# Kernel optimization log

Hardware: AMD Instinct MI355X
Metric: run time of the kernel (lower is better)

The kernel has to match this reference:

```python
import jax, jax.numpy as jnp
import numpy as np

B, S, D = 2, 2048, 2048
H = 16
Q_LORA = 1024
KV_LORA = 512
NOPE = 128
ROPE = 64
VH = 128
QK = NOPE + ROPE
EPS = 1e-3
SCALE = QK ** -0.5


def rms_norm(x, w):
    x32 = x.astype(jnp.float32)
    n = x32 * jax.lax.rsqrt(jnp.mean(x32 * x32, axis=-1, keepdims=True) + EPS)
    return w * n.astype(x.dtype)


def apply_rope(x, cos, sin):
    # x: [b, s, h, d]; cos/sin: [1, s, 1, d//2].
    # torch view_as_complex pairs consecutive elements: (x0,x1),(x2,x3),...
    xr, xi = x[..., 0::2], x[..., 1::2]
    yr = xr * cos - xi * sin
    yi = xr * sin + xi * cos
    return jnp.stack([yr, yi], axis=-1).reshape(x.shape)


def setup_inputs() -> dict:
    key = jax.random.key(0)
    ks = jax.random.split(key, 8)

    def lin(k, out, inn):
        bound = 1.0 / float(np.sqrt(inn))
        return jax.random.uniform(k, (out, inn), jnp.float32, -bound, bound)

    inv_freq = 1.0 / (10000.0 ** (np.arange(0, ROPE, 2, dtype=np.float32) / ROPE))
    ang = np.arange(S, dtype=np.float32)[:, None] * inv_freq[None, :]  # [S, ROPE/2]
    return {
        "x": jax.random.normal(ks[0], (B, S, D), jnp.float32),
        "start_pos": 0,
        "cos": jnp.asarray(np.cos(ang), jnp.float32),
        "sin": jnp.asarray(np.sin(ang), jnp.float32),
        "wq_a_w": lin(ks[1], Q_LORA, D),
        "wq_a_b": jnp.zeros((Q_LORA,), jnp.float32),
        "q_norm_w": jnp.ones((Q_LORA,), jnp.float32),
        "wq_b_w": lin(ks[2], H * QK, Q_LORA),
        "wq_b_b": jnp.zeros((H * QK,), jnp.float32),
        "wkv_a_w": lin(ks[3], KV_LORA + ROPE, D),
        "wkv_a_b": jnp.zeros((KV_LORA + ROPE,), jnp.float32),
        "kv_norm_w": jnp.ones((KV_LORA,), jnp.float32),
        "wkv_b_w": lin(ks[4], H * (NOPE + VH), KV_LORA),
        "wo_w": lin(ks[5], D, H * VH),
        "wo_b": jnp.zeros((D,), jnp.float32),
    }


def reference(x, start_pos, cos, sin, wq_a_w, wq_a_b, q_norm_w, wq_b_w, wq_b_b,
              wkv_a_w, wkv_a_b, kv_norm_w, wkv_b_w, wo_w, wo_b):
    b, s, _ = x.shape
    cos_ = cos[None, :, None, :]
    sin_ = sin[None, :, None, :]

    # q path: low-rank down-proj, RMSNorm, up-proj
    q = rms_norm(x @ wq_a_w.T + wq_a_b, q_norm_w) @ wq_b_w.T + wq_b_b
    q = q.reshape(b, s, H, QK)
    q_nope, q_pe = q[..., :NOPE], q[..., NOPE:]
    q_pe = apply_rope(q_pe, cos_, sin_)

    # kv path: joint low-rank latent + rope key
    kv_full = x @ wkv_a_w.T + wkv_a_b
    kv, k_pe = kv_full[..., :KV_LORA], kv_full[..., KV_LORA:]
    k_pe = apply_rope(k_pe[:, :, None, :], cos_, sin_)[:, :, 0, :]  # [b, t, ROPE]

    wkv_b = wkv_b_w.reshape(H, NOPE + VH, KV_LORA)
    # absorb k up-projection into q (MLA trick): q_nope -> latent space
    q_nope = jnp.einsum('bshd,hdc->bshc', q_nope, wkv_b[:, :NOPE])  # [b,s,H,KV_LORA]

    kv_c = rms_norm(kv, kv_norm_w)  # latent KV cache contents [b, t, KV_LORA]

    scores = (jnp.einsum('bshc,btc->bsht', q_nope, kv_c)
              + jnp.einsum('bshr,btr->bsht', q_pe, k_pe)) * SCALE
    # NOTE: source builds a causal mask but never adds it -> plain softmax (faithful)
    probs = jax.nn.softmax(scores.astype(jnp.float32), axis=-1).astype(x.dtype)

    o = jnp.einsum('bsht,btc->bshc', probs, kv_c)          # latent output
    o = jnp.einsum('bshc,hdc->bshd', o, wkv_b[:, NOPE:])    # v up-projection
    return o.reshape(b, s, H * VH) @ wo_w.T + wo_b
```

## Files before the change

### kernel.cpp

```cpp
#include <hip/hip_runtime.h>
#include <stdint.h>

typedef uint16_t u16;
typedef __bf16 bf16x8 __attribute__((ext_vector_type(8)));
typedef float f32x4 __attribute__((ext_vector_type(4)));
typedef u16 u16x8 __attribute__((ext_vector_type(8)));

#define EPS 1e-3f
#define SCALE_F 0.07216878364870323f
#define THR_RAW 110.0f

__device__ __forceinline__ float bf2f(u16 u) {
    union { uint32_t i; float f; } v; v.i = ((uint32_t)u) << 16; return v.f;
}
__device__ __forceinline__ u16 f2bf(float f) {
    union { float f; uint32_t i; } v; v.f = f;
    uint32_t x = v.i;
    return (u16)((x + 0x7fffu + ((x >> 16) & 1u)) >> 16);
}

__device__ __forceinline__ void async_cp16(const u16* g, u16* l) {
    __builtin_amdgcn_global_load_lds(
        (const __attribute__((address_space(1))) uint32_t*)g,
        (__attribute__((address_space(3))) uint32_t*)l,
        16, 0, 0);
}

struct Cvt {
    const void* src[14];
    u16* dst[14];
    long off[15];
};

__global__ __launch_bounds__(256) void cvt_kernel(Cvt c, const uint32_t* qnw_u32, long total8)
{
    const long i8 = (long)blockIdx.x * 256 + threadIdx.x;
    if (i8 >= total8) return;
    const long e = i8 * 8;
    const bool is_f32 = (qnw_u32[0] == 0x3F800000u);
    int t = 0;
    while (e >= c.off[t + 1]) ++t;
    const long local = e - c.off[t];
    u16* d = c.dst[t] + local;
    if (is_f32) {
        const float* s = (const float*)c.src[t] + local;
        const f32x4 a = *(const f32x4*)s;
        const f32x4 b = *(const f32x4*)(s + 4);
        u16x8 o;
        #pragma unroll
        for (int j = 0; j < 4; ++j) { o[j] = f2bf(a[j]); o[j + 4] = f2bf(b[j]); }
        *(u16x8*)d = o;
    } else {
        *(u16x8*)d = *(const u16x8*)((const u16*)c.src[t] + local);
    }
}

struct GemmP {
    const u16* A; const u16* B; const u16* bias; u16* C;
    int M, N, K, lda, ldb, ldc; float alpha; int c_f32;
    int z0, hcnt;
    long sAl, sAb, sAh, sBl, sBb, sBh, sCl, sCb, sCh;
    int gx, gy;
};

__device__ __forceinline__ void gemm_body(
    u16* As, u16* Bs, int bx, int by, int bz, const GemmP& p)
{
    const u16* A = p.A; const u16* B = p.B; const u16* bias = p.bias;
    u16* C = p.C;
    const int N = p.N, K = p.K, lda = p.lda, ldb = p.ldb, ldc = p.ldc;

    const int zg = p.z0 + bz;
    const int zb = zg / p.hcnt, zh = zg - zb * p.hcnt;
    A += (long)bz * p.sAl + (long)zb * p.sAb + (long)zh * p.sAh;
    B += (long)bz * p.sBl + (long)zb * p.sBb + (long)zh * p.sBh;
    C += (long)bz * p.sCl + (long)zb * p.sCb + (long)zh * p.sCh;

    const int tid  = threadIdx.x;
    const int wave = tid >> 6, lane = tid & 63;
    const int wm = (wave >> 1) << 6, wn = (wave & 1) << 6;
    const int quad = lane >> 4, r15 = lane & 15;

    const int tileM = by * 128;
    const int tileN = bx * 128;

    const u16* Ag[4]; const u16* Bg[4];
    u16* lA[4]; u16* lB[4];
    #pragma unroll
    for (int i = 0; i < 4; ++i) {
        const int cc = i * 256 + tid;
        const int rA = cc >> 3, kb = (cc & 7) << 3;
        int rB = tileN + rA; if (rB > N - 1) rB = N - 1;
        Ag[i] = A + (long)(tileM + rA) * lda + kb;
        Bg[i] = B + (long)rB * ldb + kb;
        lA[i] = &As[cc << 3];
        lB[i] = &Bs[cc << 3];
    }

    f32x4 acc[4][4] = {};

    const u16* aRd[4]; const u16* bRd[4];
    #pragma unroll
    for (int i = 0; i < 4; ++i) {
        aRd[i] = &As[(wm + i * 16 + r15) * 64 + quad * 8];
        bRd[i] = &Bs[(wn + i * 16 + r15) * 64 + quad * 8];
    }

    for (int k0 = 0; k0 < K; k0 += 64) {
        #pragma unroll
        for (int i = 0; i < 4; ++i) {
            async_cp16(Ag[i], lA[i]);
            async_cp16(Bg[i], lB[i]);
            Ag[i] += 64; Bg[i] += 64;
        }
        __syncthreads();
        #pragma unroll
        for (int kk = 0; kk < 2; ++kk) {
            bf16x8 af[4], bfr[4];
            #pragma unroll
            for (int i = 0; i < 4; ++i) {
                af[i]  = *(const bf16x8*)(aRd[i] + kk * 32);
                bfr[i] = *(const bf16x8*)(bRd[i] + kk * 32);
            }
            #pragma unroll
            for (int mi = 0; mi < 4; ++mi)
                #pragma unroll
                for (int ni = 0; ni < 4; ++ni)
                    acc[mi][ni] = __builtin_amdgcn_mfma_f32_16x16x32_bf16(
                        af[mi], bfr[ni], acc[mi][ni], 0, 0, 0);
        }
        __syncthreads();
    }

    #pragma unroll
    for (int mi = 0; mi < 4; ++mi) {
        const int row = tileM + wm + mi * 16 + quad * 4;
        #pragma unroll
        for (int ni = 0; ni < 4; ++ni) {
            const int col = tileN + wn + ni * 16 + r15;
            if (col < N) {
                if (p.c_f32) {
                    const float bv = bias ? bf2f(bias[col]) : 0.f;
                    #pragma unroll
                    for (int r = 0; r < 4; ++r)
                        ((float*)C)[(long)(row + r) * ldc + col] =
                            acc[mi][ni][r] * p.alpha + bv;
                } else {
                    #pragma unroll
                    for (int r = 0; r < 4; ++r) {
                        u16 t = f2bf(acc[mi][ni][r] * p.alpha);
                        if (bias) t = f2bf(bf2f(t) + bf2f(bias[col]));
                        C[(long)(row + r) * ldc + col] = t;
                    }
                }
            }
        }
    }
}

__global__ __launch_bounds__(256) void gemm_bt_kernel(GemmP p)
{
    __shared__ u16 As[128 * 64];
    __shared__ u16 Bs[128 * 64];
    gemm_body(As, Bs, blockIdx.x, blockIdx.y, blockIdx.z, p);
}

__global__ __launch_bounds__(256) void gemm_tri_kernel(
    GemmP pa, GemmP pb, GemmP pc, int na, int nb)
{
    __shared__ u16 As[128 * 64];
    __shared__ u16 Bs[128 * 64];
    int bid = blockIdx.x;
    if (bid < na) {
        const int bx = bid % pa.gx; const int rem = bid / pa.gx;
        gemm_body(As, Bs, bx, rem % pa.gy, rem / pa.gy, pa);
    } else if (bid < na + nb) {
        bid -= na;
        const int bx = bid % pb.gx; const int rem = bid / pb.gx;
        gemm_body(As, Bs, bx, rem % pb.gy, rem / pb.gy, pb);
    } else {
        bid -= na + nb;
        const int bx = bid % pc.gx; const int rem = bid / pc.gx;
        gemm_body(As, Bs, bx, rem % pc.gy, rem / pc.gy, pc);
    }
}

#define PS 72

__global__ __launch_bounds__(256, 2) void flash_kernel(
    const u16* __restrict__ q, const u16* __restrict__ K2,
    const u16* __restrict__ Vt, u16* __restrict__ O,
    const u16* __restrict__ cosb, const u16* __restrict__ sinb)
{
    __shared__ __align__(16) u16 Ks[64 * 192];
    __shared__ __align__(16) u16 Vs[128 * 64];
    __shared__ __align__(16) u16 Ps[4][32 * PS];

    const int bid = blockIdx.x;
    const int xcd = bid & 7;
    const int idx = bid >> 3;
    const int bh  = xcd * 4 + (idx >> 4);
    const int mt  = idx & 15;
    const int b = bh >> 4, h = bh & 15;

    const int tid = threadIdx.x;
    const int wave = tid >> 6, lane = tid & 63;
    const int quad = lane >> 4, r15 = lane & 15;
    const int r7 = r15 & 7;

    const long qrow0 = (long)b * 2048 + mt * 128 + wave * 32;
    u16* myPs = Ps[wave];

    bf16x8 qf[2][6];
    #pragma unroll
    for (int mi = 0; mi < 2; ++mi) {
        const u16* qp = q + (qrow0 + mi * 16 + r15) * 3072 + h * 192 + quad * 8;
        #pragma unroll
        for (int kst = 0; kst < 4; ++kst)
            qf[mi][kst] = *(const bf16x8*)(qp + kst * 32);
        const int srow = mt * 128 + wave * 32 + mi * 16 + r15;
        #pragma unroll
        for (int kst = 4; kst < 6; ++kst) {
            const u16x8 v = *(const u16x8*)(qp + kst * 32);
            u16x8 o;
            const int jj0 = (kst - 4) * 16 + quad * 4;
            #pragma unroll
            for (int pp = 0; pp < 4; ++pp) {
                const float xr = bf2f(v[2 * pp]), xi = bf2f(v[2 * pp + 1]);
                const float c  = bf2f(cosb[(long)srow * 32 + jj0 + pp]);
                const float si = bf2f(sinb[(long)srow * 32 + jj0 + pp]);
                o[2 * pp]     = f2bf(bf2f(f2bf(xr * c))  - bf2f(f2bf(xi * si)));
                o[2 * pp + 1] = f2bf(bf2f(f2bf(xr * si)) + bf2f(f2bf(xi * c)));
            }
            qf[mi][kst] = *(const bf16x8*)&o;
        }
    }

    f32x4 Oacc[2][8] = {};
    float m_i[2][4], l_i[2][4];
    #pragma unroll
    for (int mi = 0; mi < 2; ++mi)
        #pragma unroll
        for (int r = 0; r < 4; ++r) { m_i[mi][r] = -1e30f; l_i[mi][r] = 0.f; }

    const u16* Kbh = K2 + (long)b * 2048 * 3072 + h * 192;
    const u16* Vbh = Vt + (long)bh * 128 * 2048;

    const u16* gK[6];
    #pragma unroll
    for (int i = 0; i < 6; ++i) {
        const int c = i * 256 + tid;
        const int row = c / 24, s = c - row * 24;
        gK[i] = Kbh + (long)row * 3072 + ((s ^ (row & 7)) << 3);
    }
    const u16* gV[4];
    #pragma unroll
    for (int i = 0; i < 4; ++i) {
        const int c = i * 256 + tid;
        const int d = c >> 3, s = c & 7;
        gV[i] = Vbh + (long)d * 2048 + ((s ^ (d & 7)) << 3);
    }

    #pragma unroll
    for (int i = 0; i < 6; ++i) {
        async_cp16(gK[i], &Ks[(i * 256 + tid) << 3]);
        gK[i] += 64 * 3072;
    }
    __syncthreads();

    for (int j = 0; j < 32; ++j) {
        #pragma unroll
        for (int i = 0; i < 4; ++i) {
            async_cp16(gV[i], &Vs[(i * 256 + tid) << 3]);
            gV[i] += 64;
        }

        f32x4 S[2][4] = {};
        __builtin_amdgcn_s_setprio(1);
        #pragma unroll
        for (int kst = 0; kst < 6; ++kst) {
            bf16x8 bfr[4];
            #pragma unroll
            for (int ni = 0; ni < 4; ++ni)
                bfr[ni] = *(const bf16x8*)&Ks[(ni * 16 + r15) * 192
                                              + (((kst * 4 + quad) ^ r7) << 3)];
            #pragma unroll
            for (int mi = 0; mi < 2; ++mi)
                #pragma unroll
                for (int ni = 0; ni < 4; ++ni)
                    S[mi][ni] = __builtin_amdgcn_mfma_f32_16x16x32_bf16(
                        qf[mi][kst], bfr[ni], S[mi][ni], 0, 0, 0);
        }
        __builtin_amdgcn_s_setprio(0);

        __syncthreads();

        #pragma unroll
        for (int i = 0; i < 6; ++i) {
            async_cp16(gK[i], &Ks[(i * 256 + tid) << 3]);
            gK[i] += 64 * 3072;
        }

        float tmax[2][4];
        float gmax = -1e30f;
        #pragma unroll
        for (int mi = 0; mi < 2; ++mi)
            #pragma unroll
            for (int r = 0; r < 4; ++r) {
                float t = S[mi][0][r];
                #pragma unroll
                for (int ni = 1; ni < 4; ++ni) t = fmaxf(t, S[mi][ni][r]);
                t = fmaxf(t, __shfl_xor(t, 1, 16));
                t = fmaxf(t, __shfl_xor(t, 2, 16));
                t = fmaxf(t, __shfl_xor(t, 4, 16));
                t = fmaxf(t, __shfl_xor(t, 8, 16));
                tmax[mi][r] = t;
                gmax = fmaxf(gmax, t - m_i[mi][r]);
            }
        if (!__all(gmax <= THR_RAW)) {
            #pragma unroll
            for (int mi = 0; mi < 2; ++mi)
                #pragma unroll
                for (int r = 0; r < 4; ++r) {
                    const float mnew = fmaxf(m_i[mi][r], tmax[mi][r]);
                    const float al = __expf((m_i[mi][r] - mnew) * SCALE_F);
                    m_i[mi][r] = mnew;
                    l_i[mi][r] *= al;
                    #pragma unroll
                    for (int ni = 0; ni < 8; ++ni) Oacc[mi][ni][r] *= al;
                }
        }
        #pragma unroll
        for (int mi = 0; mi < 2; ++mi)
            #pragma unroll
            for (int r = 0; r < 4; ++r) {
                const int lrow = mi * 16 + quad * 4 + r;
                const float mm = m_i[mi][r];
                float ps = 0.f;
                #pragma unroll
                for (int ni = 0; ni < 4; ++ni) {
                    const float pv = __expf((S[mi][ni][r] - mm) * SCALE_F);
                    ps += pv;
                    myPs[lrow * PS + ni * 16 + r15] = f2bf(pv);
                }
                ps += __shfl_xor(ps, 1, 16);
                ps += __shfl_xor(ps, 2, 16);
                ps += __shfl_xor(ps, 4, 16);
                ps += __shfl_xor(ps, 8, 16);
                l_i[mi][r] += ps;
            }

        __builtin_amdgcn_s_setprio(1);
        #pragma unroll
        for (int kst = 0; kst < 2; ++kst) {
            bf16x8 af[2], bv[8];
            #pragma unroll
            for (int mi = 0; mi < 2; ++mi)
                af[mi] = *(const bf16x8*)&myPs[(mi * 16 + r15) * PS
                                               + kst * 32 + quad * 8];
            #pragma unroll
            for (int ni = 0; ni < 8; ++ni)
                bv[ni] = *(const bf16x8*)&Vs[(ni * 16 + r15) * 64
                                             + (((kst * 4 + quad) ^ r7) << 3)];
            #pragma unroll
            for (int mi = 0; mi < 2; ++mi)
                #pragma unroll
                for (int ni = 0; ni < 8; ++ni)
                    Oacc[mi][ni] = __builtin_amdgcn_mfma_f32_16x16x32_bf16(
                        af[mi], bv[ni], Oacc[mi][ni], 0, 0, 0);
        }
        __builtin_amdgcn_s_setprio(0);

        __syncthreads();
    }

    #pragma unroll
    for (int mi = 0; mi < 2; ++mi)
        #pragma unroll
        for (int r = 0; r < 4; ++r) {
            const float inv = 1.f / l_i[mi][r];
            const long row = qrow0 + mi * 16 + quad * 4 + r;
            #pragma unroll
            for (int ni = 0; ni < 8; ++ni)
                O[row * 2048 + h * 128 + ni * 16 + r15] =
                    f2bf(Oacc[mi][ni][r] * inv);
        }
}

__global__ __launch_bounds__(256) void norm_kv_kernel(
    const u16* __restrict__ cosb, const u16* __restrict__ sinb,
    const u16* __restrict__ qnw, const u16* __restrict__ kvnw,
    u16* __restrict__ comb, u16* __restrict__ K2)
{
    __shared__ float sm[4];
    __shared__ u16 rp[64];
    const int bid = blockIdx.x;
    const int tid = threadIdx.x;
    if (bid < 4096) {
        u16* xr = comb + (long)bid * 1600;
        float v[4];
        float ss = 0.f;
        #pragma unroll
        for (int i = 0; i < 4; ++i) { v[i] = bf2f(xr[tid + (i << 8)]); ss += v[i] * v[i]; }
        for (int o = 32; o; o >>= 1) ss += __shfl_xor(ss, o, 64);
        if ((tid & 63) == 0) sm[tid >> 6] = ss;
        __syncthreads();
        const float rinv = rsqrtf((sm[0] + sm[1] + sm[2] + sm[3]) / 1024.f + EPS);
        #pragma unroll
        for (int i = 0; i < 4; ++i) {
            const u16 nb = f2bf(v[i] * rinv);
            xr[tid + (i << 8)] = f2bf(bf2f(qnw[tid + (i << 8)]) * bf2f(nb));
        }
    } else {
        const long bs = bid - 4096;
        const int s = (int)(bs & 2047);
        u16* io = comb + bs * 1600 + 1024;
        const float v0 = bf2f(io[tid * 2]), v1 = bf2f(io[tid * 2 + 1]);
        float ss = v0 * v0 + v1 * v1;
        for (int off = 32; off; off >>= 1) ss += __shfl_xor(ss, off, 64);
        if ((tid & 63) == 0) sm[tid >> 6] = ss;
        __syncthreads();
        const float rinv = rsqrtf((sm[0] + sm[1] + sm[2] + sm[3]) / 512.f + EPS);
        const u16 n0 = f2bf(v0 * rinv), n1 = f2bf(v1 * rinv);
        io[tid * 2]     = f2bf(bf2f(kvnw[tid * 2]) * bf2f(n0));
        io[tid * 2 + 1] = f2bf(bf2f(kvnw[tid * 2 + 1]) * bf2f(n1));
        if (tid < 32) {
            const int j = tid;
            const float xr = bf2f(io[512 + 2 * j]), xi = bf2f(io[512 + 2 * j + 1]);
            const float c = bf2f(cosb[s * 32 + j]), si = bf2f(sinb[s * 32 + j]);
            rp[2 * j]     = f2bf(bf2f(f2bf(xr * c))  - bf2f(f2bf(xi * si)));
            rp[2 * j + 1] = f2bf(bf2f(f2bf(xr * si)) + bf2f(f2bf(xi * c)));
        }
        __syncthreads();
        #pragma unroll
        for (int i = 0; i < 4; ++i) {
            const int slot = tid + (i << 8);
            const int h = slot >> 6, r = slot & 63;
            K2[bs * 3072 + h * 192 + 128 + r] = rp[r];
        }
    }
}

extern "C" void kernel_launch(void* const* d_in, const int* in_sizes, int n_in,
                              void* d_out, int out_size, void* d_ws, size_t ws_size,
                              hipStream_t stream)
{
    float* out = (float*)d_out;

    char* p = (char*)d_ws;
    auto alloc = [&](size_t elems) { u16* r = (u16*)p; p += elems * 2; return r; };
    u16* c_cos  = alloc(65536);
    u16* c_sin  = alloc(65536);
    u16* c_wqa  = alloc(2097152);
    u16* c_wkva = alloc(1179648);
    u16* c_wqab = alloc(1024);
    u16* c_wkvab= alloc(576);
    u16* c_qnw  = alloc(1024);
    u16* c_wqb  = alloc(3145728);
    u16* c_wqbb = alloc(3072);
    u16* c_kvnw = alloc(512);
    u16* c_wkvb = alloc(2097152);
    u16* c_wo   = alloc(4194304);
    u16* c_wob  = alloc(2048);
    u16* q    = alloc(4096UL * 3072);
    u16* K2   = alloc(4096UL * 3072);
    u16* O    = alloc(4096UL * 2048);
    u16* comb = alloc(4096UL * 1600);
    u16* xb = (u16*)d_out;
    u16* Vt = (u16*)d_out + 8388608;

    Cvt cv;
    const long sizes[14] = {8388608, 65536, 65536, 2097152, 1024, 1024, 3145728,
                            3072, 1179648, 576, 512, 2097152, 4194304, 2048};
    u16* dsts[14] = {xb, c_cos, c_sin, c_wqa, c_wqab, c_qnw, c_wqb, c_wqbb,
                     c_wkva, c_wkvab, c_kvnw, c_wkvb, c_wo, c_wob};
    const int srcidx[14] = {0, 2, 3, 4, 5, 6, 7, 8, 9, 10, 11, 12, 13, 14};
    long acc_off = 0;
    for (int t = 0; t < 14; ++t) {
        cv.src[t] = d_in[srcidx[t]];
        cv.dst[t] = dsts[t];
        cv.off[t] = acc_off;
        acc_off += sizes[t];
    }
    cv.off[14] = acc_off;
    const long total8 = acc_off / 8;
    cvt_kernel<<<dim3((unsigned)((total8 + 255) / 256)), dim3(256), 0, stream>>>(
        cv, (const uint32_t*)d_in[6], total8);

    auto mkp = [&](const u16* A, const u16* B, const u16* bias, u16* C,
                   int M, int N, int K, int lda, int ldb, int ldc, float alpha,
                   int c_f32, int z0, int hcnt,
                   long sAl, long sAb, long sAh,
                   long sBl, long sBb, long sBh,
                   long sCl, long sCb, long sCh) {
        GemmP g;
        g.A = A; g.B = B; g.bias = bias; g.C = C;
        g.M = M; g.N = N; g.K = K; g.lda = lda; g.ldb = ldb; g.ldc = ldc;
        g.alpha = alpha; g.c_f32 = c_f32; g.z0 = z0; g.hcnt = hcnt;
        g.sAl = sAl; g.sAb = sAb; g.sAh = sAh;
        g.sBl = sBl; g.sBb = sBb; g.sBh = sBh;
        g.sCl = sCl; g.sCb = sCb; g.sCh = sCh;
        g.gx = (N + 127) / 128; g.gy = M / 128;
        return g;
    };
    auto gemm = [&](const GemmP& g, int nz) {
        gemm_bt_kernel<<<dim3(g.gx, g.gy, nz), dim3(256), 0, stream>>>(g);
    };

    gemm(mkp(xb, c_wqa, c_wqab, comb, 4096, 1600, 2048, 2048, 2048, 1600, 1.f, 0,
             0, 1, 0, 0, 0, 0, 0, 0, 0, 0, 0), 1);
    norm_kv_kernel<<<dim3(8192), dim3(256), 0, stream>>>(
        c_cos, c_sin, c_qnw, c_kvnw, comb, K2);
    {
        GemmP pq = mkp(comb, c_wqb, c_wqbb, q,
                       4096, 3072, 1024, 1600, 1024, 3072, 1.f, 0,
                       0, 1, 0, 0, 0, 0, 0, 0, 0, 0, 0);
        GemmP pk = mkp(comb + 1024, c_wkvb, nullptr, K2,
                       4096, 128, 512, 1600, 512, 3072, 1.f, 0,
                       0, 16, 0, 0, 0, 0, 0, 256L * 512, 0, 0, 192);
        pk.gx = 1; pk.gy = 32;
        GemmP pv = mkp(c_wkvb + 128 * 512, comb + 1024, nullptr, Vt,
                       128, 2048, 512, 512, 1600, 2048, 1.f, 0,
                       0, 16,
                       0, 0, 256L * 512,
                       0, 2048L * 1600, 0,
                       0, 16L * 128 * 2048, 128L * 2048);
        pv.gx = 16; pv.gy = 1;
        gemm_tri_kernel<<<dim3(1792), dim3(256), 0, stream>>>(pq, pk, pv, 768, 512);
    }
    flash_kernel<<<dim3(512), dim3(256), 0, stream>>>(q, K2, Vt, O, c_cos, c_sin);
    gemm(mkp(O, c_wo, c_wob, (u16*)out, 4096, 2048, 2048, 2048, 2048, 2048, 1.f, 1,
             0, 1, 0, 0, 0, 0, 0, 0, 0, 0, 0), 1);
}
```

Before: 500.2 us.

## Split flash attention work across 8 waves with 16 query rows each

```diff
diff --git a/kernel.cpp b/kernel.cpp
--- a/kernel.cpp
+++ b/kernel.cpp
@@ -187,14 +187,14 @@
 
 #define PS 72
 
-__global__ __launch_bounds__(256, 2) void flash_kernel(
+__global__ __launch_bounds__(512, 4) void flash_kernel(
     const u16* __restrict__ q, const u16* __restrict__ K2,
     const u16* __restrict__ Vt, u16* __restrict__ O,
     const u16* __restrict__ cosb, const u16* __restrict__ sinb)
 {
     __shared__ __align__(16) u16 Ks[64 * 192];
     __shared__ __align__(16) u16 Vs[128 * 64];
-    __shared__ __align__(16) u16 Ps[4][32 * PS];
+    __shared__ __align__(16) u16 Ps[8][16 * PS];
 
     const int bid = blockIdx.x;
     const int xcd = bid & 7;
@@ -208,17 +208,16 @@
     const int quad = lane >> 4, r15 = lane & 15;
     const int r7 = r15 & 7;
 
-    const long qrow0 = (long)b * 2048 + mt * 128 + wave * 32;
+    const long qrow0 = (long)b * 2048 + mt * 128 + wave * 16;
     u16* myPs = Ps[wave];
 
-    bf16x8 qf[2][6];
-    #pragma unroll
-    for (int mi = 0; mi < 2; ++mi) {
-        const u16* qp = q + (qrow0 + mi * 16 + r15) * 3072 + h * 192 + quad * 8;
+    bf16x8 qf[6];
+    {
+        const u16* qp = q + (qrow0 + r15) * 3072 + h * 192 + quad * 8;
         #pragma unroll
         for (int kst = 0; kst < 4; ++kst)
-            qf[mi][kst] = *(const bf16x8*)(qp + kst * 32);
-        const int srow = mt * 128 + wave * 32 + mi * 16 + r15;
+            qf[kst] = *(const bf16x8*)(qp + kst * 32);
+        const int srow = mt * 128 + wave * 16 + r15;
         #pragma unroll
         for (int kst = 4; kst < 6; ++kst) {
             const u16x8 v = *(const u16x8*)(qp + kst * 32);
@@ -232,50 +231,48 @@
                 o[2 * pp]     = f2bf(bf2f(f2bf(xr * c))  - bf2f(f2bf(xi * si)));
                 o[2 * pp + 1] = f2bf(bf2f(f2bf(xr * si)) + bf2f(f2bf(xi * c)));
             }
-            qf[mi][kst] = *(const bf16x8*)&o;
-        }
-    }
-
-    f32x4 Oacc[2][8] = {};
-    float m_i[2][4], l_i[2][4];
-    #pragma unroll
-    for (int mi = 0; mi < 2; ++mi)
-        #pragma unroll
-        for (int r = 0; r < 4; ++r) { m_i[mi][r] = -1e30f; l_i[mi][r] = 0.f; }
+            qf[kst] = *(const bf16x8*)&o;
+        }
+    }
+
+    f32x4 Oacc[8] = {};
+    float m_i[4], l_i[4];
+    #pragma unroll
+    for (int r = 0; r < 4; ++r) { m_i[r] = -1e30f; l_i[r] = 0.f; }
 
     const u16* Kbh = K2 + (long)b * 2048 * 3072 + h * 192;
     const u16* Vbh = Vt + (long)bh * 128 * 2048;
 
-    const u16* gK[6];
-    #pragma unroll
-    for (int i = 0; i < 6; ++i) {
-        const int c = i * 256 + tid;
+    const u16* gK[3];
+    #pragma unroll
+    for (int i = 0; i < 3; ++i) {
+        const int c = i * 512 + tid;
         const int row = c / 24, s = c - row * 24;
         gK[i] = Kbh + (long)row * 3072 + ((s ^ (row & 7)) << 3);
     }
-    const u16* gV[4];
-    #pragma unroll
-    for (int i = 0; i < 4; ++i) {
-        const int c = i * 256 + tid;
+    const u16* gV[2];
+    #pragma unroll
+    for (int i = 0; i < 2; ++i) {
+        const int c = i * 512 + tid;
         const int d = c >> 3, s = c & 7;
         gV[i] = Vbh + (long)d * 2048 + ((s ^ (d & 7)) << 3);
     }
 
     #pragma unroll
-    for (int i = 0; i < 6; ++i) {
-        async_cp16(gK[i], &Ks[(i * 256 + tid) << 3]);
+    for (int i = 0; i < 3; ++i) {
+        async_cp16(gK[i], &Ks[(i * 512 + tid) << 3]);
         gK[i] += 64 * 3072;
     }
     __syncthreads();
 
     for (int j = 0; j < 32; ++j) {
         #pragma unroll
-        for (int i = 0; i < 4; ++i) {
-            async_cp16(gV[i], &Vs[(i * 256 + tid) << 3]);
+        for (int i = 0; i < 2; ++i) {
+            async_cp16(gV[i], &Vs[(i * 512 + tid) << 3]);
             gV[i] += 64;
         }
 
-        f32x4 S[2][4] = {};
+        f32x4 S[4] = {};
         __builtin_amdgcn_s_setprio(1);
         #pragma unroll
         for (int kst = 0; kst < 6; ++kst) {
@@ -285,89 +282,76 @@
                 bfr[ni] = *(const bf16x8*)&Ks[(ni * 16 + r15) * 192
                                               + (((kst * 4 + quad) ^ r7) << 3)];
             #pragma unroll
-            for (int mi = 0; mi < 2; ++mi)
+            for (int ni = 0; ni < 4; ++ni)
+                S[ni] = __builtin_amdgcn_mfma_f32_16x16x32_bf16(
+                    qf[kst], bfr[ni], S[ni], 0, 0, 0);
+        }
+        __builtin_amdgcn_s_setprio(0);
+
+        __syncthreads();
+
+        #pragma unroll
+        for (int i = 0; i < 3; ++i) {
+            async_cp16(gK[i], &Ks[(i * 512 + tid) << 3]);
+            gK[i] += 64 * 3072;
+        }
+
+        float tmax[4];
+        float gmax = -1e30f;
+        #pragma unroll
+        for (int r = 0; r < 4; ++r) {
+            float t = S[0][r];
+            #pragma unroll
+            for (int ni = 1; ni < 4; ++ni) t = fmaxf(t, S[ni][r]);
+            t = fmaxf(t, __shfl_xor(t, 1, 16));
+            t = fmaxf(t, __shfl_xor(t, 2, 16));
+            t = fmaxf(t, __shfl_xor(t, 4, 16));
+            t = fmaxf(t, __shfl_xor(t, 8, 16));
+            tmax[r] = t;
+            gmax = fmaxf(gmax, t - m_i[r]);
+        }
+        if (!__all(gmax <= THR_RAW)) {
+            #pragma unroll
+            for (int r = 0; r < 4; ++r) {
+                const float mnew = fmaxf(m_i[r], tmax[r]);
+                const float al = __expf((m_i[r] - mnew) * SCALE_F);
+                m_i[r] = mnew;
+                l_i[r] *= al;
                 #pragma unroll
-                for (int ni = 0; ni < 4; ++ni)
-                    S[mi][ni] = __builtin_amdgcn_mfma_f32_16x16x32_bf16(
-                        qf[mi][kst], bfr[ni], S[mi][ni], 0, 0, 0);
-        }
-        __builtin_amdgcn_s_setprio(0);
-
-        __syncthreads();
-
-        #pragma unroll
-        for (int i = 0; i < 6; ++i) {
-            async_cp16(gK[i], &Ks[(i * 256 + tid) << 3]);
-            gK[i] += 64 * 3072;
-        }
-
-        float tmax[2][4];
-        float gmax = -1e30f;
-        #pragma unroll
-        for (int mi = 0; mi < 2; ++mi)
-            #pragma unroll
-            for (int r = 0; r < 4; ++r) {
-                float t = S[mi][0][r];
-                #pragma unroll
-                for (int ni = 1; ni < 4; ++ni) t = fmaxf(t, S[mi][ni][r]);
-                t = fmaxf(t, __shfl_xor(t, 1, 16));
-                t = fmaxf(t, __shfl_xor(t, 2, 16));
-                t = fmaxf(t, __shfl_xor(t, 4, 16));
-                t = fmaxf(t, __shfl_xor(t, 8, 16));
-                tmax[mi][r] = t;
-                gmax = fmaxf(gmax, t - m_i[mi][r]);
+                for (int ni = 0; ni < 8; ++ni) Oacc[ni][r] *= al;
             }
-        if (!__all(gmax <= THR_RAW)) {
-            #pragma unroll
-            for (int mi = 0; mi < 2; ++mi)
-                #pragma unroll
-                for (int r = 0; r < 4; ++r) {
-                    const float mnew = fmaxf(m_i[mi][r], tmax[mi][r]);
-                    const float al = __expf((m_i[mi][r] - mnew) * SCALE_F);
-                    m_i[mi][r] = mnew;
-                    l_i[mi][r] *= al;
-                    #pragma unroll
-                    for (int ni = 0; ni < 8; ++ni) Oacc[mi][ni][r] *= al;
-                }
-        }
-        #pragma unroll
-        for (int mi = 0; mi < 2; ++mi)
-            #pragma unroll
-            for (int r = 0; r < 4; ++r) {
-                const int lrow = mi * 16 + quad * 4 + r;
-                const float mm = m_i[mi][r];
-                float ps = 0.f;
-                #pragma unroll
-                for (int ni = 0; ni < 4; ++ni) {
-                    const float pv = __expf((S[mi][ni][r] - mm) * SCALE_F);
-                    ps += pv;
-                    myPs[lrow * PS + ni * 16 + r15] = f2bf(pv);
-                }
-                ps += __shfl_xor(ps, 1, 16);
-                ps += __shfl_xor(ps, 2, 16);
-                ps += __shfl_xor(ps, 4, 16);
-                ps += __shfl_xor(ps, 8, 16);
-                l_i[mi][r] += ps;
+        }
+        #pragma unroll
+        for (int r = 0; r < 4; ++r) {
+            const int lrow = quad * 4 + r;
+            const float mm = m_i[r];
+            float ps = 0.f;
+            #pragma unroll
+            for (int ni = 0; ni < 4; ++ni) {
+                const float pv = __expf((S[ni][r] - mm) * SCALE_F);
+                ps += pv;
+                myPs[lrow * PS + ni * 16 + r15] = f2bf(pv);
             }
+            ps += __shfl_xor(ps, 1, 16);
+            ps += __shfl_xor(ps, 2, 16);
+            ps += __shfl_xor(ps, 4, 16);
+            ps += __shfl_xor(ps, 8, 16);
+            l_i[r] += ps;
+        }
 
         __builtin_amdgcn_s_setprio(1);
         #pragma unroll
         for (int kst = 0; kst < 2; ++kst) {
-            bf16x8 af[2], bv[8];
-            #pragma unroll
-            for (int mi = 0; mi < 2; ++mi)
-                af[mi] = *(const bf16x8*)&myPs[(mi * 16 + r15) * PS
-                                               + kst * 32 + quad * 8];
+            bf16x8 af, bv[8];
+            af = *(const bf16x8*)&myPs[r15 * PS + kst * 32 + quad * 8];
             #pragma unroll
             for (int ni = 0; ni < 8; ++ni)
                 bv[ni] = *(const bf16x8*)&Vs[(ni * 16 + r15) * 64
                                              + (((kst * 4 + quad) ^ r7) << 3)];
             #pragma unroll
-            for (int mi = 0; mi < 2; ++mi)
-                #pragma unroll
-                for (int ni = 0; ni < 8; ++ni)
-                    Oacc[mi][ni] = __builtin_amdgcn_mfma_f32_16x16x32_bf16(
-                        af[mi], bv[ni], Oacc[mi][ni], 0, 0, 0);
+            for (int ni = 0; ni < 8; ++ni)
+                Oacc[ni] = __builtin_amdgcn_mfma_f32_16x16x32_bf16(
+                    af, bv[ni], Oacc[ni], 0, 0, 0);
         }
         __builtin_amdgcn_s_setprio(0);
 
@@ -375,16 +359,14 @@
     }
 
     #pragma unroll
-    for (int mi = 0; mi < 2; ++mi)
-        #pragma unroll
-        for (int r = 0; r < 4; ++r) {
-            const float inv = 1.f / l_i[mi][r];
-            const long row = qrow0 + mi * 16 + quad * 4 + r;
-            #pragma unroll
-            for (int ni = 0; ni < 8; ++ni)
-                O[row * 2048 + h * 128 + ni * 16 + r15] =
-                    f2bf(Oacc[mi][ni][r] * inv);
-        }
+    for (int r = 0; r < 4; ++r) {
+        const float inv = 1.f / l_i[r];
+        const long row = qrow0 + quad * 4 + r;
+        #pragma unroll
+        for (int ni = 0; ni < 8; ++ni)
+            O[row * 2048 + h * 128 + ni * 16 + r15] =
+                f2bf(Oacc[ni][r] * inv);
+    }
 }
 
 __global__ __launch_bounds__(256) void norm_kv_kernel(
@@ -528,7 +510,7 @@
         pv.gx = 16; pv.gy = 1;
         gemm_tri_kernel<<<dim3(1792), dim3(256), 0, stream>>>(pq, pk, pv, 768, 512);
     }
-    flash_kernel<<<dim3(512), dim3(256), 0, stream>>>(q, K2, Vt, O, c_cos, c_sin);
+    flash_kernel<<<dim3(512), dim3(512), 0, stream>>>(q, K2, Vt, O, c_cos, c_sin);
     gemm(mkp(O, c_wo, c_wob, (u16*)out, 4096, 2048, 2048, 2048, 2048, 2048, 1.f, 1,
              0, 1, 0, 0, 0, 0, 0, 0, 0, 0, 0), 1);
 }
```

Result: faster. 486.1 us (-2.8%).
